# Kernel tuning notes

Hardware: AMD Instinct MI355X
Metric: run time of the kernel (lower is better)

The kernel has to match this reference:

```python
import jax, jax.numpy as jnp
import numpy as np

B, S, D = 4, 4096, 2048
DQ = D // 4          # router hidden
DF = 4 * D           # layer_fn FFN hidden
CAPACITY = 0.125


def setup_inputs() -> dict:
    key = jax.random.key(0)
    ks = jax.random.split(key, 5)
    sc = 0.02
    return {
        "x":   jax.random.normal(ks[0], (B, S, D), jnp.float32),
        "Wr1": jax.random.normal(ks[1], (D, DQ), jnp.float32) * sc,
        "br1": jnp.zeros((DQ,), jnp.float32),
        "Wr2": jax.random.normal(ks[2], (DQ, 1), jnp.float32) * sc,
        "br2": jnp.zeros((1,), jnp.float32),
        "Wf1": jax.random.normal(ks[3], (D, DF), jnp.float32) * sc,
        "bf1": jnp.zeros((DF,), jnp.float32),
        "Wf2": jax.random.normal(ks[4], (DF, D), jnp.float32) * sc,
        "bf2": jnp.zeros((D,), jnp.float32),
    }


def reference(x, Wr1, br1, Wr2, br2, Wf1, bf1, Wf2, bf2):
    b, s, d = x.shape
    k = max(1, int(CAPACITY * s))

    # router: Linear -> ReLU -> Linear -> squeeze(-1)
    h = jax.nn.relu(jnp.einsum("bsd,dq->bsq", x, Wr1) + br1)
    scores = (jnp.einsum("bsq,qo->bso", h, Wr2) + br2)[..., 0]   # [B, S]

    # top-k token selection per batch row
    topk_scores, topk_idx = jax.lax.top_k(scores, k)             # [B, k]

    # gather selected tokens
    sel = jnp.take_along_axis(x, topk_idx[..., None], axis=1)    # [B, k, D]

    # layer_fn: standard FFN (D -> 4D -> D) on selected tokens only
    proc = jnp.einsum("bkf,fd->bkd",
                      jax.nn.relu(jnp.einsum("bkd,df->bkf", sel, Wf1) + bf1),
                      Wf2) + bf2                                 # [B, k, D]

    # scatter processed tokens back into a copy of x
    batch_idx = jnp.arange(b)[:, None]                           # [B, 1]
    output = x.at[batch_idx, topk_idx].set(proc)                 # [B, S, D]

    mask = jnp.zeros((b, s), dtype=bool).at[batch_idx, topk_idx].set(True)
    return output, mask
```

## Files before the change

kernel.cpp:

```cpp
#include <hip/hip_runtime.h>

#define B_    4
#define S_    4096
#define D_    2048
#define DQ_   512
#define DF_   8192
#define KSEL_ 512
#define M_    (B_ * S_)
#define MS_   (B_ * KSEL_)

typedef __attribute__((ext_vector_type(8))) short bf16x8;
typedef __attribute__((ext_vector_type(4))) float f32x4;
typedef __attribute__((address_space(3))) void as3_void;
typedef const __attribute__((address_space(1))) void as1_cvoid;

__device__ __forceinline__ unsigned short f2bf(float f) {
    unsigned u = __float_as_uint(f);
    u += 0x7FFFu + ((u >> 16) & 1u);
    return (unsigned short)(u >> 16);
}
__device__ __forceinline__ float bf2f(unsigned short h) {
    return __uint_as_float(((unsigned)h) << 16);
}

__device__ __forceinline__ void gload16(const void* g, void* l) {
    __builtin_amdgcn_global_load_lds((as1_cvoid*)g, (as3_void*)l, 16, 0, 0);
}

__global__ void split_copy_kernel(const float* __restrict__ x,
                                  unsigned short* __restrict__ xh,
                                  unsigned short* __restrict__ xl,
                                  float* __restrict__ out, int n8) {
    int i = blockIdx.x * blockDim.x + threadIdx.x;
    int stride = gridDim.x * blockDim.x;
    for (; i < n8; i += stride) {
        float4 a = ((const float4*)x)[2 * i];
        float4 b = ((const float4*)x)[2 * i + 1];
        ((float4*)out)[2 * i]     = a;
        ((float4*)out)[2 * i + 1] = b;
        float v[8] = {a.x, a.y, a.z, a.w, b.x, b.y, b.z, b.w};
        unsigned short hi[8], lo[8];
#pragma unroll
        for (int j = 0; j < 8; j++) {
            hi[j] = f2bf(v[j]);
            lo[j] = f2bf(v[j] - bf2f(hi[j]));
        }
        *(uint4*)(xh + (size_t)i * 8) = *(const uint4*)hi;
        *(uint4*)(xl + (size_t)i * 8) = *(const uint4*)lo;
    }
}

__global__ void wsplit_kernel(const float* __restrict__ W,
                              unsigned short* __restrict__ whiT,
                              unsigned short* __restrict__ wloT) {
    __shared__ float tile[32][33];
    int tx = threadIdx.x, ty = threadIdx.y;
    int n0 = blockIdx.x * 32, k0 = blockIdx.y * 32;
#pragma unroll
    for (int j = 0; j < 4; j++)
        tile[ty + j * 8][tx] = W[(size_t)(k0 + ty + j * 8) * DQ_ + n0 + tx];
    __syncthreads();
#pragma unroll
    for (int j = 0; j < 4; j++) {
        float v = tile[tx][ty + j * 8];
        unsigned short hi = f2bf(v);
        unsigned short lo = f2bf(v - bf2f(hi));
        size_t row = (size_t)(n0 + ty + j * 8) * D_;
        whiT[row + k0 + tx] = hi;
        wloT[row + k0 + tx] = lo;
    }
}

__global__ void transpose_bf16_kernel(const float* __restrict__ in,
                                      unsigned short* __restrict__ out,
                                      int R, int C) {
    __shared__ float tile[32][33];
    int tx = threadIdx.x, ty = threadIdx.y;
    int c0 = blockIdx.x * 32, r0 = blockIdx.y * 32;
#pragma unroll
    for (int j = 0; j < 4; j++)
        tile[ty + j * 8][tx] = in[(size_t)(r0 + ty + j * 8) * C + c0 + tx];
    __syncthreads();
#pragma unroll
    for (int j = 0; j < 4; j++)
        out[(size_t)(c0 + ty + j * 8) * R + r0 + tx] = f2bf(tile[tx][ty + j * 8]);
}

__global__ __launch_bounds__(256) void router_mfma(const unsigned short* __restrict__ xh,
                                                   const unsigned short* __restrict__ xl,
                                                   const unsigned short* __restrict__ whiT,
                                                   const unsigned short* __restrict__ wloT,
                                                   const float* __restrict__ bias,
                                                   float* __restrict__ H) {
    __shared__ unsigned short Ah[128 * 32];
    __shared__ unsigned short Al[128 * 32];
    __shared__ unsigned short Bh[128 * 32];
    __shared__ unsigned short Bl[128 * 32];
    const int t = threadIdx.x;
    const int w = t >> 6, l = t & 63;
    const int m0 = blockIdx.x * 128, n0 = blockIdx.y * 128;
    const int wm = (w >> 1) * 64, wn = (w & 1) * 64;

    f32x4 acc[4][4];
    const f32x4 z = {0.f, 0.f, 0.f, 0.f};
#pragma unroll
    for (int i = 0; i < 4; i++)
#pragma unroll
        for (int j = 0; j < 4; j++) acc[i][j] = z;

    const int ra = t >> 2;
    const int ca = (((t & 3) ^ ((t >> 3) & 3)) * 8);
    const unsigned short* gAh0 = xh + (size_t)(m0 + ra) * D_ + ca;
    const unsigned short* gAh1 = xh + (size_t)(m0 + 64 + ra) * D_ + ca;
    const unsigned short* gAl0 = xl + (size_t)(m0 + ra) * D_ + ca;
    const unsigned short* gAl1 = xl + (size_t)(m0 + 64 + ra) * D_ + ca;
    const unsigned short* gBh0 = whiT + (size_t)(n0 + ra) * D_ + ca;
    const unsigned short* gBh1 = whiT + (size_t)(n0 + 64 + ra) * D_ + ca;
    const unsigned short* gBl0 = wloT + (size_t)(n0 + ra) * D_ + ca;
    const unsigned short* gBl1 = wloT + (size_t)(n0 + 64 + ra) * D_ + ca;
    char* lAh = (char*)Ah + w * 1024;
    char* lAl = (char*)Al + w * 1024;
    char* lBh = (char*)Bh + w * 1024;
    char* lBl = (char*)Bl + w * 1024;

    const int ro = (((l >> 4) ^ ((l >> 1) & 3)) * 8);

    for (int k0 = 0; k0 < D_; k0 += 32) {
        gload16(gAh0 + k0, lAh);
        gload16(gAh1 + k0, lAh + 4096);
        gload16(gAl0 + k0, lAl);
        gload16(gAl1 + k0, lAl + 4096);
        gload16(gBh0 + k0, lBh);
        gload16(gBh1 + k0, lBh + 4096);
        gload16(gBl0 + k0, lBl);
        gload16(gBl1 + k0, lBl + 4096);
        __syncthreads();
        bf16x8 ah[4], al[4], bh[4], bl[4];
#pragma unroll
        for (int i = 0; i < 4; i++) {
            int ar = (wm + i * 16 + (l & 15)) * 32 + ro;
            int br = (wn + i * 16 + (l & 15)) * 32 + ro;
            ah[i] = *(const bf16x8*)(Ah + ar);
            al[i] = *(const bf16x8*)(Al + ar);
            bh[i] = *(const bf16x8*)(Bh + br);
            bl[i] = *(const bf16x8*)(Bl + br);
        }
#pragma unroll
        for (int i = 0; i < 4; i++)
#pragma unroll
            for (int j = 0; j < 4; j++) {
                acc[i][j] = __builtin_amdgcn_mfma_f32_16x16x32_bf16(ah[i], bh[j], acc[i][j], 0, 0, 0);
                acc[i][j] = __builtin_amdgcn_mfma_f32_16x16x32_bf16(ah[i], bl[j], acc[i][j], 0, 0, 0);
                acc[i][j] = __builtin_amdgcn_mfma_f32_16x16x32_bf16(al[i], bh[j], acc[i][j], 0, 0, 0);
            }
        __syncthreads();
    }
#pragma unroll
    for (int i = 0; i < 4; i++) {
        int mbase = m0 + wm + i * 16 + (l >> 4) * 4;
#pragma unroll
        for (int j = 0; j < 4; j++) {
            int n = n0 + wn + j * 16 + (l & 15);
            float bv = bias[n];
#pragma unroll
            for (int q = 0; q < 4; q++)
                H[(size_t)(mbase + q) * DQ_ + n] = fmaxf(acc[i][j][q] + bv, 0.f);
        }
    }
}

__global__ void score_kernel(const float* __restrict__ H, const float* __restrict__ Wr2,
                             const float* __restrict__ br2, float* __restrict__ scores) {
    int wv = threadIdx.x >> 6, l = threadIdx.x & 63;
    int tok = blockIdx.x * 4 + wv;
    const float* hrow = H + (size_t)tok * DQ_;
    float4 a0 = ((const float4*)hrow)[l];
    float4 a1 = ((const float4*)hrow)[64 + l];
    float4 w0 = ((const float4*)Wr2)[l];
    float4 w1 = ((const float4*)Wr2)[64 + l];
    float s = a0.x * w0.x + a0.y * w0.y + a0.z * w0.z + a0.w * w0.w
            + a1.x * w1.x + a1.y * w1.y + a1.z * w1.z + a1.w * w1.w;
#pragma unroll
    for (int off = 32; off >= 1; off >>= 1) s += __shfl_xor(s, off);
    if (l == 0) scores[tok] = s + br2[0];
}

__global__ __launch_bounds__(1024) void topk_kernel(const float* __restrict__ scores,
                                                    int* __restrict__ sel_idx,
                                                    float* __restrict__ maskF) {
    __shared__ unsigned long long keys[S_];
    __shared__ unsigned char flags[S_];
    int b = blockIdx.x, t = threadIdx.x;
    for (int i = t; i < S_; i += 1024) {
        float f = scores[b * S_ + i];
        unsigned u = __float_as_uint(f);
        u = (u & 0x80000000u) ? ~u : (u | 0x80000000u);
        keys[i] = ((unsigned long long)u << 32) | (unsigned)(S_ - 1 - i);
        flags[i] = 0;
    }
    __syncthreads();
    for (int k = 2; k <= S_; k <<= 1)
        for (int j = k >> 1; j > 0; j >>= 1) {
            for (int i = t; i < S_; i += 1024) {
                int l = i ^ j;
                if (l > i) {
                    unsigned long long a = keys[i], c = keys[l];
                    bool up = ((i & k) == 0);
                    if (up ? (a > c) : (a < c)) { keys[i] = c; keys[l] = a; }
                }
            }
            __syncthreads();
        }
    for (int i = t; i < KSEL_; i += 1024) {
        unsigned long long kk = keys[S_ - KSEL_ + i];
        int s = (S_ - 1) - (int)(kk & 0xFFFFFFFFu);
        sel_idx[b * KSEL_ + i] = s;
        flags[s] = 1;
    }
    __syncthreads();
    for (int i = t; i < S_; i += 1024)
        maskF[b * S_ + i] = flags[i] ? 1.0f : 0.0f;
}

__global__ void gather_kernel(const float* __restrict__ x, const int* __restrict__ sel_idx,
                              unsigned short* __restrict__ sel) {
    int jrow = blockIdx.x;
    int b = jrow >> 9;
    int tok = sel_idx[jrow];
    const float* src = x + ((size_t)(b * S_ + tok)) * D_;
    int t = threadIdx.x;
    float4 v0 = ((const float4*)src)[2 * t];
    float4 v1 = ((const float4*)src)[2 * t + 1];
    unsigned p0 = (unsigned)f2bf(v0.x) | ((unsigned)f2bf(v0.y) << 16);
    unsigned p1 = (unsigned)f2bf(v0.z) | ((unsigned)f2bf(v0.w) << 16);
    unsigned p2 = (unsigned)f2bf(v1.x) | ((unsigned)f2bf(v1.y) << 16);
    unsigned p3 = (unsigned)f2bf(v1.z) | ((unsigned)f2bf(v1.w) << 16);
    *(uint4*)(sel + (size_t)jrow * D_ + t * 8) = make_uint4(p0, p1, p2, p3);
}

#define STAGEAB(bufp, ktX) do {                                                   \
    const unsigned short* a_ = gA + (size_t)(ktX) * 64;                           \
    const unsigned short* b_ = gB + (size_t)(ktX) * 64;                           \
    char* la_ = (char*)(&lds[bufp][0][0]) + w * 1024;                             \
    char* lb_ = (char*)(&lds[bufp][1][0]) + w * 1024;                             \
    gload16(a_,                      la_);                                        \
    gload16(a_ +  64 * (size_t)K,    la_ + 8192);                                 \
    gload16(a_ + 128 * (size_t)K,    la_ + 16384);                                \
    gload16(a_ + 192 * (size_t)K,    la_ + 24576);                                \
    gload16(b_,                      lb_);                                        \
    gload16(b_ +  64 * (size_t)K,    lb_ + 8192);                                 \
    gload16(b_ + 128 * (size_t)K,    lb_ + 16384);                                \
    gload16(b_ + 192 * (size_t)K,    lb_ + 24576);                                \
  } while (0)

#define PHASE256(mh, kk, LOADB) do {                                              \
    const int sw_ = (((kk) * 4 + (l >> 4)) ^ (l & 7)) * 8;                        \
    if (LOADB) {                                                                  \
      _Pragma("unroll")                                                           \
      for (int n = 0; n < 4; n++)                                                 \
        bfr[n] = *(const bf16x8*)(LB + (wc * 64 + n * 16 + (l & 15)) * 64 + sw_); \
    }                                                                             \
    _Pragma("unroll")                                                             \
    for (int m = 0; m < 4; m++)                                                   \
      afr[m] = *(const bf16x8*)(LA + (wr * 128 + (mh) * 64 + m * 16 + (l & 15)) * 64 + sw_); \
    __builtin_amdgcn_s_barrier();                                                 \
    __builtin_amdgcn_s_setprio(1);                                                \
    _Pragma("unroll")                                                             \
    for (int m = 0; m < 4; m++)                                                   \
      _Pragma("unroll")                                                           \
      for (int n = 0; n < 4; n++)                                                 \
        acc[(mh) * 4 + m][n] =                                                    \
            __builtin_amdgcn_mfma_f32_16x16x32_bf16(afr[m], bfr[n], acc[(mh) * 4 + m][n], 0, 0, 0); \
    __builtin_amdgcn_s_setprio(0);                                                \
    __builtin_amdgcn_s_barrier();                                                 \
  } while (0)

__global__ __launch_bounds__(512) void mfma_gemm256(const unsigned short* __restrict__ A,
                                                    const unsigned short* __restrict__ Bt,
                                                    int M, int N, int K, int kspan,
                                                    const float* __restrict__ bias,
                                                    unsigned short* __restrict__ Cbf,
                                                    float* __restrict__ partial,
                                                    int epi) {
    __shared__ unsigned short lds[2][2][256 * 64];
    const int t = threadIdx.x;
    const int w = t >> 6, l = t & 63;
    const int m0 = blockIdx.y * 256, n0 = blockIdx.x * 256;
    const int wr = w >> 2, wc = w & 3;
    const int kbeg = blockIdx.z * kspan;
    const int NT = kspan / 64;

    f32x4 acc[8][4];
    const f32x4 zz = {0.f, 0.f, 0.f, 0.f};
#pragma unroll
    for (int m = 0; m < 8; m++)
#pragma unroll
        for (int n = 0; n < 4; n++) acc[m][n] = zz;

    const int srow = t >> 3;
    const int sch8 = (((t & 7) ^ ((t >> 3) & 7)) * 8);
    const unsigned short* gA = A + (size_t)(m0 + srow) * K + kbeg + sch8;
    const unsigned short* gB = Bt + (size_t)(n0 + srow) * K + kbeg + sch8;

    STAGEAB(0, 0);
    STAGEAB(1, 1);

    bf16x8 afr[4], bfr[4];
    for (int kt = 0; kt < NT; ++kt) {
        if (kt + 1 < NT) { asm volatile("s_waitcnt vmcnt(8)" ::: "memory"); }
        else             { asm volatile("s_waitcnt vmcnt(0)" ::: "memory"); }
        __builtin_amdgcn_s_barrier();
        __builtin_amdgcn_sched_barrier(0);
        const int cur = kt & 1;
        const unsigned short* LA = &lds[cur][0][0];
        const unsigned short* LB = &lds[cur][1][0];
        PHASE256(0, 0, 1);
        PHASE256(1, 0, 0);
        PHASE256(0, 1, 1);
        PHASE256(1, 1, 0);
        __builtin_amdgcn_sched_barrier(0);
        if (kt + 2 < NT) STAGEAB(cur, kt + 2);
    }

    if (epi == 0) {
#pragma unroll
        for (int m = 0; m < 8; m++) {
            int rowb = m0 + wr * 128 + m * 16 + (l >> 4) * 4;
#pragma unroll
            for (int n = 0; n < 4; n++) {
                int col = n0 + wc * 64 + n * 16 + (l & 15);
                float bv = bias[col];
#pragma unroll
                for (int q = 0; q < 4; q++) {
                    float v = fmaxf(acc[m][n][q] + bv, 0.f);
                    Cbf[(size_t)(rowb + q) * N + col] = f2bf(v);
                }
            }
        }
    } else {
        float* pseg = partial + (size_t)blockIdx.z * M * N;
#pragma unroll
        for (int m = 0; m < 8; m++) {
            int rowb = m0 + wr * 128 + m * 16 + (l >> 4) * 4;
#pragma unroll
            for (int n = 0; n < 4; n++) {
                int col = n0 + wc * 64 + n * 16 + (l & 15);
#pragma unroll
                for (int q = 0; q < 4; q++)
                    pseg[(size_t)(rowb + q) * N + col] = acc[m][n][q];
            }
        }
    }
}

__global__ void reduce_scatter_kernel(const float* __restrict__ partial,
                                      const float* __restrict__ bias,
                                      const int* __restrict__ sel_idx,
                                      float* __restrict__ out) {
    int m = blockIdx.x;
    int t = threadIdx.x;
    int brow = m >> 9;
    int tok = sel_idx[m];
    float* orow = out + ((size_t)(brow * S_ + tok)) * D_;
    const float* p0 = partial + (size_t)m * D_;
    const size_t seg = (size_t)MS_ * D_;
#pragma unroll
    for (int r = 0; r < 2; r++) {
        int c = (t + r * 256) * 4;
        float4 v0 = *(const float4*)(p0 + c);
        float4 v1 = *(const float4*)(p0 + seg + c);
        float4 v2 = *(const float4*)(p0 + 2 * seg + c);
        float4 v3 = *(const float4*)(p0 + 3 * seg + c);
        float4 bv = *(const float4*)(bias + c);
        float4 o;
        o.x = v0.x + v1.x + v2.x + v3.x + bv.x;
        o.y = v0.y + v1.y + v2.y + v3.y + bv.y;
        o.z = v0.z + v1.z + v2.z + v3.z + bv.z;
        o.w = v0.w + v1.w + v2.w + v3.w + bv.w;
        *(float4*)(orow + c) = o;
    }
}

extern "C" void kernel_launch(void* const* d_in, const int* in_sizes, int n_in,
                              void* d_out, int out_size, void* d_ws, size_t ws_size,
                              hipStream_t stream) {
    const float* x   = (const float*)d_in[0];
    const float* Wr1 = (const float*)d_in[1];
    const float* br1 = (const float*)d_in[2];
    const float* Wr2 = (const float*)d_in[3];
    const float* br2 = (const float*)d_in[4];
    const float* Wf1 = (const float*)d_in[5];
    const float* bf1 = (const float*)d_in[6];
    const float* Wf2 = (const float*)d_in[7];
    const float* bf2 = (const float*)d_in[8];
    float* out = (float*)d_out;
    char* ws = (char*)d_ws;

    unsigned short* xh   = (unsigned short*)(ws);
    unsigned short* xl   = (unsigned short*)(ws + (64u << 20));
    float* h             = (float*)(ws + (128u << 20));
    unsigned short* whiT = (unsigned short*)(ws + (160u << 20));
    unsigned short* wloT = (unsigned short*)(ws + (162u << 20));
    float* scores        = (float*)(ws + (168u << 20));
    int* sel_idx         = (int*)(ws + (169u << 20));
    float* partial       = (float*)(ws);
    unsigned short* w1t  = (unsigned short*)(ws + (64u << 20));
    unsigned short* w2t  = (unsigned short*)(ws + (96u << 20));
    unsigned short* h1   = (unsigned short*)(ws + (128u << 20));
    unsigned short* sel  = (unsigned short*)(ws + (160u << 20));
    float* maskF         = out + (size_t)B_ * S_ * D_;

    (void)in_sizes; (void)n_in; (void)out_size; (void)ws_size;

    split_copy_kernel<<<2048, 256, 0, stream>>>(x, xh, xl, out, (M_ * D_) / 8);
    wsplit_kernel<<<dim3(DQ_ / 32, D_ / 32), dim3(32, 8), 0, stream>>>(Wr1, whiT, wloT);
    router_mfma<<<dim3(M_ / 128, DQ_ / 128), 256, 0, stream>>>(xh, xl, whiT, wloT, br1, h);
    score_kernel<<<M_ / 4, 256, 0, stream>>>(h, Wr2, br2, scores);
    topk_kernel<<<B_, 1024, 0, stream>>>(scores, sel_idx, maskF);
    gather_kernel<<<MS_, 256, 0, stream>>>(x, sel_idx, sel);
    transpose_bf16_kernel<<<dim3(DF_ / 32, D_ / 32), dim3(32, 8), 0, stream>>>(Wf1, w1t, D_, DF_);
    transpose_bf16_kernel<<<dim3(D_ / 32, DF_ / 32), dim3(32, 8), 0, stream>>>(Wf2, w2t, DF_, D_);
    mfma_gemm256<<<dim3(DF_ / 256, MS_ / 256, 1), 512, 0, stream>>>(
        sel, w1t, MS_, DF_, D_, D_, bf1, h1, nullptr, 0);
    mfma_gemm256<<<dim3(D_ / 256, MS_ / 256, 4), 512, 0, stream>>>(
        h1, w2t, MS_, D_, DF_, DF_ / 4, nullptr, nullptr, partial, 1);
    reduce_scatter_kernel<<<MS_, 256, 0, stream>>>(partial, bf2, sel_idx, out);
}
```

Baseline: 462.4 us.

## Fuse router score projection into router GEMM with double-buffered 256x128 tiles

The router GEMM now folds bias, ReLU and the Wr2 dot product into its epilogue, writing eight per-column-slice partial scores instead of the full 16384x512 hidden matrix. The separate score kernel is removed and top-k sums the eight partials plus br2. The GEMM also moves to 512-thread blocks with 256x128 tiles, double-buffered LDS prefetch using explicit vmcnt waits, and setprio around the MFMA phases. This cuts the hidden-activation write and read-back plus one launch, at the cost of more LDS per block and a different summation order for the scores, which could change top-k ties.

```diff
diff --git a/kernel.cpp b/kernel.cpp
--- a/kernel.cpp
+++ b/kernel.cpp
@@ -86,113 +86,134 @@
         out[(size_t)(c0 + ty + j * 8) * R + r0 + tx] = f2bf(tile[tx][ty + j * 8]);
 }
 
-__global__ __launch_bounds__(256) void router_mfma(const unsigned short* __restrict__ xh,
+#define RSTAGE(bufp, ktX) do {                                              \
+    const size_t ko_ = (size_t)(ktX) * 32;                                  \
+    char* laH_ = (char*)(&sA[bufp][0][0]) + w * 1024;                       \
+    char* laL_ = (char*)(&sA[bufp][1][0]) + w * 1024;                       \
+    char* lbH_ = (char*)(&sB[bufp][0][0]) + w * 1024;                       \
+    char* lbL_ = (char*)(&sB[bufp][1][0]) + w * 1024;                       \
+    gload16(gAh + ko_,                 laH_);                               \
+    gload16(gAh + 128 * D_ + ko_,      laH_ + 8192);                        \
+    gload16(gAl + ko_,                 laL_);                               \
+    gload16(gAl + 128 * D_ + ko_,      laL_ + 8192);                        \
+    gload16(gBh + ko_,                 lbH_);                               \
+    gload16(gBl + ko_,                 lbL_);                               \
+  } while (0)
+
+#define RPHASE(AF, BF) do {                                                 \
+    __builtin_amdgcn_s_barrier();                                           \
+    __builtin_amdgcn_s_setprio(1);                                          \
+    _Pragma("unroll")                                                       \
+    for (int m = 0; m < 4; m++)                                             \
+      _Pragma("unroll")                                                     \
+      for (int n = 0; n < 4; n++)                                           \
+        acc[m][n] = __builtin_amdgcn_mfma_f32_16x16x32_bf16(AF[m], BF[n], acc[m][n], 0, 0, 0); \
+    __builtin_amdgcn_s_setprio(0);                                          \
+    __builtin_amdgcn_s_barrier();                                           \
+  } while (0)
+
+__global__ __launch_bounds__(512) void router_mfma(const unsigned short* __restrict__ xh,
                                                    const unsigned short* __restrict__ xl,
                                                    const unsigned short* __restrict__ whiT,
                                                    const unsigned short* __restrict__ wloT,
-                                                   const float* __restrict__ bias,
-                                                   float* __restrict__ H) {
-    __shared__ unsigned short Ah[128 * 32];
-    __shared__ unsigned short Al[128 * 32];
-    __shared__ unsigned short Bh[128 * 32];
-    __shared__ unsigned short Bl[128 * 32];
+                                                   const float* __restrict__ br1,
+                                                   const float* __restrict__ Wr2,
+                                                   float* __restrict__ pscore) {
+    __shared__ unsigned short sA[2][2][256 * 32];
+    __shared__ unsigned short sB[2][2][128 * 32];
     const int t = threadIdx.x;
     const int w = t >> 6, l = t & 63;
-    const int m0 = blockIdx.x * 128, n0 = blockIdx.y * 128;
-    const int wm = (w >> 1) * 64, wn = (w & 1) * 64;
+    const int m0 = blockIdx.x * 256, n0 = blockIdx.y * 128;
+    const int wr = w >> 1, wc = w & 1;
 
     f32x4 acc[4][4];
-    const f32x4 z = {0.f, 0.f, 0.f, 0.f};
-#pragma unroll
-    for (int i = 0; i < 4; i++)
-#pragma unroll
-        for (int j = 0; j < 4; j++) acc[i][j] = z;
-
-    const int ra = t >> 2;
-    const int ca = (((t & 3) ^ ((t >> 3) & 3)) * 8);
-    const unsigned short* gAh0 = xh + (size_t)(m0 + ra) * D_ + ca;
-    const unsigned short* gAh1 = xh + (size_t)(m0 + 64 + ra) * D_ + ca;
-    const unsigned short* gAl0 = xl + (size_t)(m0 + ra) * D_ + ca;
-    const unsigned short* gAl1 = xl + (size_t)(m0 + 64 + ra) * D_ + ca;
-    const unsigned short* gBh0 = whiT + (size_t)(n0 + ra) * D_ + ca;
-    const unsigned short* gBh1 = whiT + (size_t)(n0 + 64 + ra) * D_ + ca;
-    const unsigned short* gBl0 = wloT + (size_t)(n0 + ra) * D_ + ca;
-    const unsigned short* gBl1 = wloT + (size_t)(n0 + 64 + ra) * D_ + ca;
-    char* lAh = (char*)Ah + w * 1024;
-    char* lAl = (char*)Al + w * 1024;
-    char* lBh = (char*)Bh + w * 1024;
-    char* lBl = (char*)Bl + w * 1024;
-
-    const int ro = (((l >> 4) ^ ((l >> 1) & 3)) * 8);
-
-    for (int k0 = 0; k0 < D_; k0 += 32) {
-        gload16(gAh0 + k0, lAh);
-        gload16(gAh1 + k0, lAh + 4096);
-        gload16(gAl0 + k0, lAl);
-        gload16(gAl1 + k0, lAl + 4096);
-        gload16(gBh0 + k0, lBh);
-        gload16(gBh1 + k0, lBh + 4096);
-        gload16(gBl0 + k0, lBl);
-        gload16(gBl1 + k0, lBl + 4096);
-        __syncthreads();
-        bf16x8 ah[4], al[4], bh[4], bl[4];
-#pragma unroll
-        for (int i = 0; i < 4; i++) {
-            int ar = (wm + i * 16 + (l & 15)) * 32 + ro;
-            int br = (wn + i * 16 + (l & 15)) * 32 + ro;
-            ah[i] = *(const bf16x8*)(Ah + ar);
-            al[i] = *(const bf16x8*)(Al + ar);
-            bh[i] = *(const bf16x8*)(Bh + br);
-            bl[i] = *(const bf16x8*)(Bl + br);
-        }
-#pragma unroll
-        for (int i = 0; i < 4; i++)
-#pragma unroll
-            for (int j = 0; j < 4; j++) {
-                acc[i][j] = __builtin_amdgcn_mfma_f32_16x16x32_bf16(ah[i], bh[j], acc[i][j], 0, 0, 0);
-                acc[i][j] = __builtin_amdgcn_mfma_f32_16x16x32_bf16(ah[i], bl[j], acc[i][j], 0, 0, 0);
-                acc[i][j] = __builtin_amdgcn_mfma_f32_16x16x32_bf16(al[i], bh[j], acc[i][j], 0, 0, 0);
+    const f32x4 zz = {0.f, 0.f, 0.f, 0.f};
+#pragma unroll
+    for (int m = 0; m < 4; m++)
+#pragma unroll
+        for (int n = 0; n < 4; n++) acc[m][n] = zz;
+
+    const int srow = t >> 2;
+    const int sch8 = (((t & 3) ^ ((t >> 2) & 3)) * 8);
+    const unsigned short* gAh = xh + (size_t)(m0 + srow) * D_ + sch8;
+    const unsigned short* gAl = xl + (size_t)(m0 + srow) * D_ + sch8;
+    const unsigned short* gBh = whiT + (size_t)(n0 + srow) * D_ + sch8;
+    const unsigned short* gBl = wloT + (size_t)(n0 + srow) * D_ + sch8;
+
+    RSTAGE(0, 0);
+    RSTAGE(1, 1);
+
+    const int fro = ((l >> 4) ^ (l & 3)) * 8;
+    bf16x8 ah[4], al[4], bh[4], bl[4];
+
+    for (int kt = 0; kt < 64; ++kt) {
+        if (kt + 1 < 64) { asm volatile("s_waitcnt vmcnt(6)" ::: "memory"); }
+        else             { asm volatile("s_waitcnt vmcnt(0)" ::: "memory"); }
+        __builtin_amdgcn_s_barrier();
+        __builtin_amdgcn_sched_barrier(0);
+        const int cur = kt & 1;
+        const unsigned short* LAh = &sA[cur][0][0];
+        const unsigned short* LAl = &sA[cur][1][0];
+        const unsigned short* LBh = &sB[cur][0][0];
+        const unsigned short* LBl = &sB[cur][1][0];
+#pragma unroll
+        for (int f = 0; f < 4; f++) {
+            int ar = (wr * 64 + f * 16 + (l & 15)) * 32 + fro;
+            int br = (wc * 64 + f * 16 + (l & 15)) * 32 + fro;
+            ah[f] = *(const bf16x8*)(LAh + ar);
+            bh[f] = *(const bf16x8*)(LBh + br);
+        }
+        RPHASE(ah, bh);
+#pragma unroll
+        for (int f = 0; f < 4; f++)
+            bl[f] = *(const bf16x8*)(LBl + (wc * 64 + f * 16 + (l & 15)) * 32 + fro);
+        RPHASE(ah, bl);
+#pragma unroll
+        for (int f = 0; f < 4; f++)
+            al[f] = *(const bf16x8*)(LAl + (wr * 64 + f * 16 + (l & 15)) * 32 + fro);
+        RPHASE(al, bh);
+        __builtin_amdgcn_sched_barrier(0);
+        if (kt + 2 < 64) RSTAGE(cur, kt + 2);
+    }
+
+    float br1v[4], wr2v[4];
+#pragma unroll
+    for (int nf = 0; nf < 4; nf++) {
+        int col = n0 + wc * 64 + nf * 16 + (l & 15);
+        br1v[nf] = br1[col];
+        wr2v[nf] = Wr2[col];
+    }
+#pragma unroll
+    for (int mf = 0; mf < 4; mf++)
+#pragma unroll
+        for (int q = 0; q < 4; q++) {
+            float s = 0.f;
+#pragma unroll
+            for (int nf = 0; nf < 4; nf++)
+                s += fmaxf(acc[mf][nf][q] + br1v[nf], 0.f) * wr2v[nf];
+#pragma unroll
+            for (int off = 8; off >= 1; off >>= 1)
+                s += __shfl_xor(s, off);
+            if ((l & 15) == 0) {
+                int row = m0 + wr * 64 + mf * 16 + (l >> 4) * 4 + q;
+                pscore[(size_t)(blockIdx.y * 2 + wc) * M_ + row] = s;
             }
-        __syncthreads();
-    }
-#pragma unroll
-    for (int i = 0; i < 4; i++) {
-        int mbase = m0 + wm + i * 16 + (l >> 4) * 4;
-#pragma unroll
-        for (int j = 0; j < 4; j++) {
-            int n = n0 + wn + j * 16 + (l & 15);
-            float bv = bias[n];
-#pragma unroll
-            for (int q = 0; q < 4; q++)
-                H[(size_t)(mbase + q) * DQ_ + n] = fmaxf(acc[i][j][q] + bv, 0.f);
-        }
-    }
-}
-
-__global__ void score_kernel(const float* __restrict__ H, const float* __restrict__ Wr2,
-                             const float* __restrict__ br2, float* __restrict__ scores) {
-    int wv = threadIdx.x >> 6, l = threadIdx.x & 63;
-    int tok = blockIdx.x * 4 + wv;
-    const float* hrow = H + (size_t)tok * DQ_;
-    float4 a0 = ((const float4*)hrow)[l];
-    float4 a1 = ((const float4*)hrow)[64 + l];
-    float4 w0 = ((const float4*)Wr2)[l];
-    float4 w1 = ((const float4*)Wr2)[64 + l];
-    float s = a0.x * w0.x + a0.y * w0.y + a0.z * w0.z + a0.w * w0.w
-            + a1.x * w1.x + a1.y * w1.y + a1.z * w1.z + a1.w * w1.w;
-#pragma unroll
-    for (int off = 32; off >= 1; off >>= 1) s += __shfl_xor(s, off);
-    if (l == 0) scores[tok] = s + br2[0];
-}
-
-__global__ __launch_bounds__(1024) void topk_kernel(const float* __restrict__ scores,
+        }
+}
+
+__global__ __launch_bounds__(1024) void topk_kernel(const float* __restrict__ pscore,
+                                                    const float* __restrict__ br2,
                                                     int* __restrict__ sel_idx,
                                                     float* __restrict__ maskF) {
     __shared__ unsigned long long keys[S_];
     __shared__ unsigned char flags[S_];
     int b = blockIdx.x, t = threadIdx.x;
+    float bb = br2[0];
     for (int i = t; i < S_; i += 1024) {
-        float f = scores[b * S_ + i];
+        int m = b * S_ + i;
+        float f = bb;
+#pragma unroll
+        for (int s8 = 0; s8 < 8; s8++) f += pscore[(size_t)s8 * M_ + m];
         unsigned u = __float_as_uint(f);
         u = (u & 0x80000000u) ? ~u : (u | 0x80000000u);
         keys[i] = ((unsigned long long)u << 32) | (unsigned)(S_ - 1 - i);
@@ -398,10 +419,9 @@
 
     unsigned short* xh   = (unsigned short*)(ws);
     unsigned short* xl   = (unsigned short*)(ws + (64u << 20));
-    float* h             = (float*)(ws + (128u << 20));
     unsigned short* whiT = (unsigned short*)(ws + (160u << 20));
     unsigned short* wloT = (unsigned short*)(ws + (162u << 20));
-    float* scores        = (float*)(ws + (168u << 20));
+    float* pscore        = (float*)(ws + (168u << 20));
     int* sel_idx         = (int*)(ws + (169u << 20));
     float* partial       = (float*)(ws);
     unsigned short* w1t  = (unsigned short*)(ws + (64u << 20));
@@ -414,9 +434,9 @@
 
     split_copy_kernel<<<2048, 256, 0, stream>>>(x, xh, xl, out, (M_ * D_) / 8);
     wsplit_kernel<<<dim3(DQ_ / 32, D_ / 32), dim3(32, 8), 0, stream>>>(Wr1, whiT, wloT);
-    router_mfma<<<dim3(M_ / 128, DQ_ / 128), 256, 0, stream>>>(xh, xl, whiT, wloT, br1, h);
-    score_kernel<<<M_ / 4, 256, 0, stream>>>(h, Wr2, br2, scores);
-    topk_kernel<<<B_, 1024, 0, stream>>>(scores, sel_idx, maskF);
+    router_mfma<<<dim3(M_ / 256, DQ_ / 128), 512, 0, stream>>>(
+        xh, xl, whiT, wloT, br1, Wr2, pscore);
+    topk_kernel<<<B_, 1024, 0, stream>>>(pscore, br2, sel_idx, maskF);
     gather_kernel<<<MS_, 256, 0, stream>>>(x, sel_idx, sel);
     transpose_bf16_kernel<<<dim3(DF_ / 32, D_ / 32), dim3(32, 8), 0, stream>>>(Wf1, w1t, D_, DF_);
     transpose_bf16_kernel<<<dim3(D_ / 32, DF_ / 32), dim3(32, 8), 0, stream>>>(Wf2, w2t, DF_, D_);
```

Result: slower. 500.2 us (+8.2%).
